# Kernel optimization log

Hardware: AMD Instinct MI355X
Metric: run time of the kernel (lower is better)

Reference implementation:

```python
import jax, jax.numpy as jnp
import numpy as np

B, T_OUT, C, L = 8, 8, 64, 1024  # batch, temporal channels, spatial channels (=in_channels), time steps


def setup_inputs() -> dict:
    key = jax.random.key(0)
    ks = jax.random.split(key, 7)
    s = 1.0 / np.sqrt(C)  # conv1d default init scale
    return {
        "x": jax.random.normal(ks[0], (B, T_OUT, C, L), dtype=jnp.float32),
        "Wq": jax.random.uniform(ks[1], (C, C), jnp.float32, -s, s),
        "bq": jax.random.uniform(ks[2], (C,), jnp.float32, -s, s),
        "Wk": jax.random.uniform(ks[3], (C, C), jnp.float32, -s, s),
        "bk": jax.random.uniform(ks[4], (C,), jnp.float32, -s, s),
        "Wv": jax.random.uniform(ks[5], (C, C), jnp.float32, -s, s),
        "bv": jax.random.uniform(ks[6], (C,), jnp.float32, -s, s),
    }


def reference(x, Wq, bq, Wk, bk, Wv, bv):
    b, t, c, l = x.shape
    xr = x.reshape(b * t, c, l)  # [BT, C, L]
    # 1x1 Conv1d == per-timestep linear over channels
    q = jnp.einsum('oc,bcl->bol', Wq, xr) + bq[:, None]
    k = jnp.einsum('oc,bcl->bol', Wk, xr) + bk[:, None]
    v = jnp.einsum('oc,bcl->bol', Wv, xr) + bv[:, None]
    # scores[b, i, j] = sum_c q[b, c, i] * k[b, c, j]  -> [BT, L, L]
    scores = jnp.einsum('bci,bcj->bij', q, k)
    weights = jax.nn.softmax(scores, axis=-1)
    # out[b, i, c] = sum_j weights[b, i, j] * v[b, c, j]
    out = jnp.einsum('bij,bcj->bic', weights, v)
    out = jnp.transpose(out, (0, 2, 1))  # [BT, C, L]
    return out.reshape(b, t, c, l)
```

## Files before the change

### kernel.cpp

```cpp
#include <hip/hip_runtime.h>

#define CC 64
#define LL 1024
#define LOG2E 1.44269504f

typedef unsigned short u16;
typedef unsigned int u32;
typedef __attribute__((ext_vector_type(8))) short short8;
typedef __attribute__((ext_vector_type(4))) float floatx4;

static __device__ __forceinline__ u16 f2b(float f) {
  return (u16)((__float_as_uint(f) + 0x8000u) >> 16);
}
static __device__ __forceinline__ u32 pk2(float a, float b) {
  return ((__float_as_uint(a) + 0x8000u) >> 16) |
         ((__float_as_uint(b) + 0x8000u) & 0xffff0000u);
}
static __device__ __forceinline__ u32 pk2t(float a, float b) {
  return __builtin_amdgcn_perm(__float_as_uint(b), __float_as_uint(a), 0x07060302u);
}
static __device__ __forceinline__ short8 mk8(u32 a, u32 b, u32 c, u32 d) {
  union { u32 u[4]; short8 s; } t;
  t.u[0] = a; t.u[1] = b; t.u[2] = c; t.u[3] = d;
  return t.s;
}

__global__ __launch_bounds__(256) void w_prep(
    const float* __restrict__ Wq, const float* __restrict__ bq,
    const float* __restrict__ Wk, const float* __restrict__ bk,
    const float* __restrict__ Wv, const float* __restrict__ bv,
    u16* __restrict__ whi, float* __restrict__ bsc)
{
  const int idx = blockIdx.x * 256 + threadIdx.x;
  const int m = idx >> 12;
  const float* W = (m == 0) ? Wq : (m == 1) ? Wk : Wv;
  const float w = W[idx & 4095] * ((m == 0) ? LOG2E : 1.0f);
  whi[idx] = f2b(w);
  if (blockIdx.x == 0 && threadIdx.x < 192)
    bsc[threadIdx.x] = (threadIdx.x < 64) ? bq[threadIdx.x] * LOG2E
                     : (threadIdx.x < 128) ? bk[threadIdx.x - 64] : bv[threadIdx.x - 128];
}

__global__ __launch_bounds__(256) void qkv_kernel(
    const float* __restrict__ x,
    const u16* __restrict__ whi, const float* __restrict__ bsc,
    u16* __restrict__ qT, u16* __restrict__ kT, u16* __restrict__ vO)
{
  __shared__ __align__(16) u16 tbuf_s[4 * 16 * 72];

  const int tid  = threadIdx.x;
  const int wave = tid >> 6;
  const int lane = tid & 63;
  const int l16  = lane & 15;
  const int quad = lane >> 4;

  const int bt = blockIdx.x & 63;
  const int l0 = (blockIdx.x >> 6) << 6;
  const int l  = l0 + wave * 16 + l16;

  const float* xb = x + (size_t)bt * CC * LL + l;
  float xv0[8], xv1[8];
  #pragma unroll
  for (int e = 0; e < 8; ++e) {
    xv0[e] = xb[(size_t)(quad * 8 + e) * LL];
    xv1[e] = xb[(size_t)(quad * 8 + 32 + e) * LL];
  }
  const short8 xh0 = mk8(pk2(xv0[0], xv0[1]), pk2(xv0[2], xv0[3]),
                         pk2(xv0[4], xv0[5]), pk2(xv0[6], xv0[7]));
  const short8 xh1 = mk8(pk2(xv1[0], xv1[1]), pk2(xv1[2], xv1[3]),
                         pk2(xv1[4], xv1[5]), pk2(xv1[6], xv1[7]));

  u16* tb = tbuf_s + wave * 1152;

  #pragma unroll
  for (int ot = 0; ot < 12; ++ot) {
    const int m = ot >> 2;
    const int off = (m << 12) + (((ot & 3) * 16 + l16) << 6) + quad * 8;
    const short8 ah0 = *(const short8*)(whi + off);
    const short8 ah1 = *(const short8*)(whi + off + 32);

    floatx4 acc = (floatx4){0.f, 0.f, 0.f, 0.f};
    acc = __builtin_amdgcn_mfma_f32_16x16x32_bf16(ah0, xh0, acc, 0, 0, 0);
    acc = __builtin_amdgcn_mfma_f32_16x16x32_bf16(ah1, xh1, acc, 0, 0, 0);

    const float4 bb = *(const float4*)(bsc + ot * 16 + quad * 4);
    float ov[4];
    ov[0] = acc[0] + bb.x; ov[1] = acc[1] + bb.y;
    ov[2] = acc[2] + bb.z; ov[3] = acc[3] + bb.w;

    if (ot < 8) {
      uint2 pv;
      pv.x = pk2(ov[0], ov[1]);
      pv.y = pk2(ov[2], ov[3]);
      *(uint2*)(tb + l16 * 72 + (ot & 3) * 16 + quad * 4) = pv;
      if ((ot & 3) == 3) {
        asm volatile("" ::: "memory");
        u16* gdst = ((ot < 4) ? qT : kT) + ((size_t)(bt * LL + l0 + wave * 16)) * CC;
        const int rr = lane >> 3;
        const int c8 = (lane & 7) * 8;
        #pragma unroll
        for (int s2 = 0; s2 < 2; ++s2) {
          const int row = s2 * 8 + rr;
          uint4 val = *(const uint4*)(tb + row * 72 + c8);
          *(uint4*)(gdst + row * CC + c8) = val;
        }
        asm volatile("" ::: "memory");
      }
    } else {
      const int ob = (ot - 8) * 16 + quad * 4;
      u16* vdst = vO + ((size_t)(bt * CC + ob)) * LL + l0 + wave * 16 + l16;
      #pragma unroll
      for (int r = 0; r < 4; ++r)
        vdst[(size_t)r * LL] = f2b(ov[r]);
    }
  }
}

__global__ __launch_bounds__(256) void attn_kernel(
    const u16* __restrict__ qT, const u16* __restrict__ kT,
    const u16* __restrict__ vB, float* __restrict__ out)
{
  __shared__ __align__(16) u16 smem[18432];
  const int tid  = threadIdx.x;
  const int wave = tid >> 6;
  const int lane = tid & 63;
  const int l16  = lane & 15;
  const int quad = lane >> 4;

  const int bt    = blockIdx.x & 63;
  const int chunk = blockIdx.x >> 6;
  const int i0w   = (chunk << 6) + (wave << 4);

  const u16* kbase = kT + (size_t)bt * LL * CC;
  const u16* vbase = vB + (size_t)bt * CC * LL;

  short8 qf[2];
  {
    const u16* qr = qT + (size_t)bt * LL * CC + (size_t)(i0w + l16) * CC + quad * 8;
    qf[0] = *(const short8*)(qr);
    qf[1] = *(const short8*)(qr + 32);
  }

  floatx4 O[4];
  #pragma unroll
  for (int cf = 0; cf < 4; ++cf)
    O[cf] = (floatx4){0.f, 0.f, 0.f, 0.f};
  float lsA = 0.f, lsB = 0.f;

  const int r_st = tid >> 2;
  const int c_st = (tid & 3) << 4;
  const int sr = (r_st & 0x20) | ((r_st & 4) << 2) | ((r_st & 0x18) >> 1) | (r_st & 3);

  {
    uint4 k0 = *(const uint4*)(kbase + (size_t)r_st * CC + c_st);
    uint4 k1 = *(const uint4*)(kbase + (size_t)r_st * CC + c_st + 8);
    uint4 v0 = *(const uint4*)(vbase + (size_t)r_st * LL + c_st);
    uint4 v1 = *(const uint4*)(vbase + (size_t)r_st * LL + c_st + 8);
    *(uint4*)(smem + sr * 72 + c_st)              = k0;
    *(uint4*)(smem + sr * 72 + c_st + 8)          = k1;
    *(uint4*)(smem + 4608 + r_st * 72 + c_st)     = v0;
    *(uint4*)(smem + 4608 + r_st * 72 + c_st + 8) = v1;
  }
  __syncthreads();

  for (int it = 0; it < 16; ++it) {
    u16* ktc = smem + (it & 1) * 9216;
    u16* vtc = ktc + 4608;

    uint4 rk0, rk1, rv0, rv1;
    if (it < 15) {
      const int jb = (it + 1) << 6;
      rk0 = *(const uint4*)(kbase + (size_t)(jb + r_st) * CC + c_st);
      rk1 = *(const uint4*)(kbase + (size_t)(jb + r_st) * CC + c_st + 8);
      rv0 = *(const uint4*)(vbase + (size_t)r_st * LL + jb + c_st);
      rv1 = *(const uint4*)(vbase + (size_t)r_st * LL + jb + c_st + 8);
    }

    floatx4 S[4];
    __builtin_amdgcn_s_setprio(1);
    #pragma unroll
    for (int jt = 0; jt < 4; ++jt) {
      const u16* ka = ktc + (jt * 16 + l16) * 72 + quad * 8;
      const short8 a0 = *(const short8*)(ka);
      const short8 a1 = *(const short8*)(ka + 32);
      floatx4 acc = (floatx4){0.f, 0.f, 0.f, 0.f};
      acc = __builtin_amdgcn_mfma_f32_16x16x32_bf16(a0, qf[0], acc, 0, 0, 0);
      acc = __builtin_amdgcn_mfma_f32_16x16x32_bf16(a1, qf[1], acc, 0, 0, 0);
      S[jt] = acc;
    }
    __builtin_amdgcn_s_setprio(0);

    short8 v0f[4], v1f[4];
    #pragma unroll
    for (int cf = 0; cf < 4; ++cf) {
      const u16* va = vtc + (cf * 16 + l16) * 72 + quad * 8;
      v0f[cf] = *(const short8*)(va);
      v1f[cf] = *(const short8*)(va + 32);
    }

    uint2 pp[4];
    #pragma unroll
    for (int jt = 0; jt < 4; ++jt) {
      const float e0 = __builtin_amdgcn_exp2f(S[jt][0]);
      const float e1 = __builtin_amdgcn_exp2f(S[jt][1]);
      const float e2 = __builtin_amdgcn_exp2f(S[jt][2]);
      const float e3 = __builtin_amdgcn_exp2f(S[jt][3]);
      lsA += e0 + e1;
      lsB += e2 + e3;
      pp[jt].x = pk2t(e0, e1);
      pp[jt].y = pk2t(e2, e3);
    }

    __builtin_amdgcn_s_setprio(1);
    {
      const short8 pa0 = mk8(pp[0].x, pp[0].y, pp[1].x, pp[1].y);
      const short8 pa1 = mk8(pp[2].x, pp[2].y, pp[3].x, pp[3].y);
      #pragma unroll
      for (int cf = 0; cf < 4; ++cf) {
        O[cf] = __builtin_amdgcn_mfma_f32_16x16x32_bf16(pa0, v0f[cf], O[cf], 0, 0, 0);
        O[cf] = __builtin_amdgcn_mfma_f32_16x16x32_bf16(pa1, v1f[cf], O[cf], 0, 0, 0);
      }
    }
    __builtin_amdgcn_s_setprio(0);

    if (it < 15) {
      u16* ktn = smem + ((it + 1) & 1) * 9216;
      *(uint4*)(ktn + sr * 72 + c_st)              = rk0;
      *(uint4*)(ktn + sr * 72 + c_st + 8)          = rk1;
      *(uint4*)(ktn + 4608 + r_st * 72 + c_st)     = rv0;
      *(uint4*)(ktn + 4608 + r_st * 72 + c_st + 8) = rv1;
    }
    __syncthreads();
  }

  float lsum = lsA + lsB;
  lsum += __shfl_xor(lsum, 16, 64);
  lsum += __shfl_xor(lsum, 32, 64);

  __syncthreads();
  float* of = (float*)smem + wave * 1280;
  #pragma unroll
  for (int r = 0; r < 4; ++r) {
    const float rl = __builtin_amdgcn_rcpf(__shfl(lsum, quad * 4 + r, 64));
    #pragma unroll
    for (int cf = 0; cf < 4; ++cf)
      O[cf][r] *= rl;
  }
  asm volatile("" ::: "memory");
  #pragma unroll
  for (int cf = 0; cf < 4; ++cf)
    #pragma unroll
    for (int r = 0; r < 4; ++r)
      of[(cf * 16 + l16) * 20 + quad * 4 + r] = O[cf][r];
  asm volatile("" ::: "memory");
  {
    float* ob = out + ((size_t)bt * CC) * LL + i0w;
    #pragma unroll
    for (int rr = 0; rr < 4; ++rr) {
      const int c = rr * 16 + l16;
      float4 val = *(const float4*)(of + c * 20 + quad * 4);
      *(float4*)(ob + (size_t)c * LL + quad * 4) = val;
    }
  }
  asm volatile("" ::: "memory");
}

extern "C" void kernel_launch(void* const* d_in, const int* in_sizes, int n_in,
                              void* d_out, int out_size, void* d_ws, size_t ws_size,
                              hipStream_t stream) {
  const float* x  = (const float*)d_in[0];
  const float* Wq = (const float*)d_in[1];
  const float* bq = (const float*)d_in[2];
  const float* Wk = (const float*)d_in[3];
  const float* bk = (const float*)d_in[4];
  const float* Wv = (const float*)d_in[5];
  const float* bv = (const float*)d_in[6];
  float* out = (float*)d_out;

  u16* qTp = (u16*)d_ws;
  u16* kTp = qTp + (size_t)64 * LL * CC;
  u16* vp  = kTp + (size_t)64 * LL * CC;
  u16* whi = vp  + (size_t)64 * LL * CC;
  float* bsc = (float*)(whi + 3 * 64 * 64);

  w_prep<<<48, 256, 0, stream>>>(Wq, bq, Wk, bk, Wv, bv, whi, bsc);
  qkv_kernel<<<1024, 256, 0, stream>>>(x, whi, bsc, qTp, kTp, vp);
  attn_kernel<<<1024, 256, 0, stream>>>(qTp, kTp, vp, out);
}
```

Baseline: 123.5 us.

## Fuse QKV projection into attention kernel, recomputing K/V tiles per block

Merges the projection and attention kernels: each 512-thread block projects its own Q rows and recomputes K and V tiles from x directly into shared memory while iterating over keys, prefetching the next x tile. This removes the bf16 Q/K/V workspace writes and reads and one kernel launch. In exchange, K/V projection is redundantly recomputed by every block sharing a batch slice, and x is re-read multiple times with strided fp32 loads.

```diff
diff --git a/kernel.cpp b/kernel.cpp
--- a/kernel.cpp
+++ b/kernel.cpp
@@ -41,12 +41,12 @@
                      : (threadIdx.x < 128) ? bk[threadIdx.x - 64] : bv[threadIdx.x - 128];
 }
 
-__global__ __launch_bounds__(256) void qkv_kernel(
+__global__ __launch_bounds__(512) void fused_kernel(
     const float* __restrict__ x,
     const u16* __restrict__ whi, const float* __restrict__ bsc,
-    u16* __restrict__ qT, u16* __restrict__ kT, u16* __restrict__ vO)
+    float* __restrict__ out)
 {
-  __shared__ __align__(16) u16 tbuf_s[4 * 16 * 72];
+  __shared__ __align__(16) u16 smem[20480];
 
   const int tid  = threadIdx.x;
   const int wave = tid >> 6;
@@ -54,91 +54,47 @@
   const int l16  = lane & 15;
   const int quad = lane >> 4;
 
-  const int bt = blockIdx.x & 63;
-  const int l0 = (blockIdx.x >> 6) << 6;
-  const int l  = l0 + wave * 16 + l16;
-
-  const float* xb = x + (size_t)bt * CC * LL + l;
-  float xv0[8], xv1[8];
-  #pragma unroll
-  for (int e = 0; e < 8; ++e) {
-    xv0[e] = xb[(size_t)(quad * 8 + e) * LL];
-    xv1[e] = xb[(size_t)(quad * 8 + 32 + e) * LL];
-  }
-  const short8 xh0 = mk8(pk2(xv0[0], xv0[1]), pk2(xv0[2], xv0[3]),
-                         pk2(xv0[4], xv0[5]), pk2(xv0[6], xv0[7]));
-  const short8 xh1 = mk8(pk2(xv1[0], xv1[1]), pk2(xv1[2], xv1[3]),
-                         pk2(xv1[4], xv1[5]), pk2(xv1[6], xv1[7]));
-
-  u16* tb = tbuf_s + wave * 1152;
-
-  #pragma unroll
-  for (int ot = 0; ot < 12; ++ot) {
-    const int m = ot >> 2;
-    const int off = (m << 12) + (((ot & 3) * 16 + l16) << 6) + quad * 8;
-    const short8 ah0 = *(const short8*)(whi + off);
-    const short8 ah1 = *(const short8*)(whi + off + 32);
-
-    floatx4 acc = (floatx4){0.f, 0.f, 0.f, 0.f};
-    acc = __builtin_amdgcn_mfma_f32_16x16x32_bf16(ah0, xh0, acc, 0, 0, 0);
-    acc = __builtin_amdgcn_mfma_f32_16x16x32_bf16(ah1, xh1, acc, 0, 0, 0);
-
-    const float4 bb = *(const float4*)(bsc + ot * 16 + quad * 4);
-    float ov[4];
-    ov[0] = acc[0] + bb.x; ov[1] = acc[1] + bb.y;
-    ov[2] = acc[2] + bb.z; ov[3] = acc[3] + bb.w;
-
-    if (ot < 8) {
+  const int bt  = blockIdx.x & 63;
+  const int ih  = blockIdx.x >> 6;
+  const int i0w = (ih << 7) + (wave << 4);
+
+  const int jt  = wave & 3;
+  const int ot0 = (wave >> 2) << 1;
+
+  const float* xbt = x + (size_t)bt * CC * LL;
+
+  short8 qf0, qf1;
+  {
+    const float* xq = xbt + i0w + l16;
+    float qx[16];
+    #pragma unroll
+    for (int e = 0; e < 8; ++e) {
+      qx[e]     = xq[(size_t)(quad * 8 + e) * LL];
+      qx[8 + e] = xq[(size_t)(quad * 8 + 32 + e) * LL];
+    }
+    const short8 qxh0 = mk8(pk2(qx[0], qx[1]), pk2(qx[2], qx[3]),
+                            pk2(qx[4], qx[5]), pk2(qx[6], qx[7]));
+    const short8 qxh1 = mk8(pk2(qx[8], qx[9]), pk2(qx[10], qx[11]),
+                            pk2(qx[12], qx[13]), pk2(qx[14], qx[15]));
+    u16* tb = smem + 9216 + wave * 1152;
+    #pragma unroll
+    for (int ot = 0; ot < 4; ++ot) {
+      const int off = ((ot * 16 + l16) << 6) + quad * 8;
+      const short8 ah0 = *(const short8*)(whi + off);
+      const short8 ah1 = *(const short8*)(whi + off + 32);
+      floatx4 acc = (floatx4){0.f, 0.f, 0.f, 0.f};
+      acc = __builtin_amdgcn_mfma_f32_16x16x32_bf16(ah0, qxh0, acc, 0, 0, 0);
+      acc = __builtin_amdgcn_mfma_f32_16x16x32_bf16(ah1, qxh1, acc, 0, 0, 0);
+      const float4 bb = *(const float4*)(bsc + ot * 16 + quad * 4);
       uint2 pv;
-      pv.x = pk2(ov[0], ov[1]);
-      pv.y = pk2(ov[2], ov[3]);
-      *(uint2*)(tb + l16 * 72 + (ot & 3) * 16 + quad * 4) = pv;
-      if ((ot & 3) == 3) {
-        asm volatile("" ::: "memory");
-        u16* gdst = ((ot < 4) ? qT : kT) + ((size_t)(bt * LL + l0 + wave * 16)) * CC;
-        const int rr = lane >> 3;
-        const int c8 = (lane & 7) * 8;
-        #pragma unroll
-        for (int s2 = 0; s2 < 2; ++s2) {
-          const int row = s2 * 8 + rr;
-          uint4 val = *(const uint4*)(tb + row * 72 + c8);
-          *(uint4*)(gdst + row * CC + c8) = val;
-        }
-        asm volatile("" ::: "memory");
-      }
-    } else {
-      const int ob = (ot - 8) * 16 + quad * 4;
-      u16* vdst = vO + ((size_t)(bt * CC + ob)) * LL + l0 + wave * 16 + l16;
-      #pragma unroll
-      for (int r = 0; r < 4; ++r)
-        vdst[(size_t)r * LL] = f2b(ov[r]);
-    }
-  }
-}
-
-__global__ __launch_bounds__(256) void attn_kernel(
-    const u16* __restrict__ qT, const u16* __restrict__ kT,
-    const u16* __restrict__ vB, float* __restrict__ out)
-{
-  __shared__ __align__(16) u16 smem[18432];
-  const int tid  = threadIdx.x;
-  const int wave = tid >> 6;
-  const int lane = tid & 63;
-  const int l16  = lane & 15;
-  const int quad = lane >> 4;
-
-  const int bt    = blockIdx.x & 63;
-  const int chunk = blockIdx.x >> 6;
-  const int i0w   = (chunk << 6) + (wave << 4);
-
-  const u16* kbase = kT + (size_t)bt * LL * CC;
-  const u16* vbase = vB + (size_t)bt * CC * LL;
-
-  short8 qf[2];
-  {
-    const u16* qr = qT + (size_t)bt * LL * CC + (size_t)(i0w + l16) * CC + quad * 8;
-    qf[0] = *(const short8*)(qr);
-    qf[1] = *(const short8*)(qr + 32);
+      pv.x = pk2(acc[0] + bb.x, acc[1] + bb.y);
+      pv.y = pk2(acc[2] + bb.z, acc[3] + bb.w);
+      *(uint2*)(tb + l16 * 72 + ot * 16 + quad * 4) = pv;
+    }
+    asm volatile("" ::: "memory");
+    qf0 = *(const short8*)(tb + l16 * 72 + quad * 8);
+    qf1 = *(const short8*)(tb + l16 * 72 + quad * 8 + 32);
+    asm volatile("" ::: "memory");
   }
 
   floatx4 O[4];
@@ -147,68 +103,106 @@
     O[cf] = (floatx4){0.f, 0.f, 0.f, 0.f};
   float lsA = 0.f, lsB = 0.f;
 
-  const int r_st = tid >> 2;
-  const int c_st = (tid & 3) << 4;
-  const int sr = (r_st & 0x20) | ((r_st & 4) << 2) | ((r_st & 0x18) >> 1) | (r_st & 3);
+  const int jloc = jt * 16 + l16;
+  const int srow = (jloc & 32) | ((jloc & 4) << 2) | ((jloc & 24) >> 1) | (jloc & 3);
+
+  auto proj = [&](const float (&px)[16], u16* Kb, u16* Vb) {
+    const short8 xh0 = mk8(pk2(px[0], px[1]), pk2(px[2], px[3]),
+                           pk2(px[4], px[5]), pk2(px[6], px[7]));
+    const short8 xh1 = mk8(pk2(px[8], px[9]), pk2(px[10], px[11]),
+                           pk2(px[12], px[13]), pk2(px[14], px[15]));
+    #pragma unroll
+    for (int o2 = 0; o2 < 2; ++o2) {
+      const int ot = ot0 + o2;
+      {
+        const int off = 4096 + ((ot * 16 + l16) << 6) + quad * 8;
+        const short8 ah0 = *(const short8*)(whi + off);
+        const short8 ah1 = *(const short8*)(whi + off + 32);
+        floatx4 acc = (floatx4){0.f, 0.f, 0.f, 0.f};
+        acc = __builtin_amdgcn_mfma_f32_16x16x32_bf16(ah0, xh0, acc, 0, 0, 0);
+        acc = __builtin_amdgcn_mfma_f32_16x16x32_bf16(ah1, xh1, acc, 0, 0, 0);
+        const float4 bb = *(const float4*)(bsc + 64 + ot * 16 + quad * 4);
+        uint2 pv;
+        pv.x = pk2(acc[0] + bb.x, acc[1] + bb.y);
+        pv.y = pk2(acc[2] + bb.z, acc[3] + bb.w);
+        *(uint2*)(Kb + srow * 72 + ot * 16 + quad * 4) = pv;
+      }
+      {
+        const int off = 8192 + ((ot * 16 + l16) << 6) + quad * 8;
+        const short8 ah0 = *(const short8*)(whi + off);
+        const short8 ah1 = *(const short8*)(whi + off + 32);
+        floatx4 acc = (floatx4){0.f, 0.f, 0.f, 0.f};
+        acc = __builtin_amdgcn_mfma_f32_16x16x32_bf16(ah0, xh0, acc, 0, 0, 0);
+        acc = __builtin_amdgcn_mfma_f32_16x16x32_bf16(ah1, xh1, acc, 0, 0, 0);
+        const float4 bb = *(const float4*)(bsc + 128 + ot * 16 + quad * 4);
+        #pragma unroll
+        for (int r = 0; r < 4; ++r) {
+          const float ov = acc[r] + ((const float*)&bb)[r];
+          Vb[(ot * 16 + quad * 4 + r) * 72 + jloc] = f2b(ov);
+        }
+      }
+    }
+  };
 
   {
-    uint4 k0 = *(const uint4*)(kbase + (size_t)r_st * CC + c_st);
-    uint4 k1 = *(const uint4*)(kbase + (size_t)r_st * CC + c_st + 8);
-    uint4 v0 = *(const uint4*)(vbase + (size_t)r_st * LL + c_st);
-    uint4 v1 = *(const uint4*)(vbase + (size_t)r_st * LL + c_st + 8);
-    *(uint4*)(smem + sr * 72 + c_st)              = k0;
-    *(uint4*)(smem + sr * 72 + c_st + 8)          = k1;
-    *(uint4*)(smem + 4608 + r_st * 72 + c_st)     = v0;
-    *(uint4*)(smem + 4608 + r_st * 72 + c_st + 8) = v1;
+    float p0[16];
+    const float* xp = xbt + jt * 16 + l16;
+    #pragma unroll
+    for (int e = 0; e < 8; ++e) {
+      p0[e]     = xp[(size_t)(quad * 8 + e) * LL];
+      p0[8 + e] = xp[(size_t)(quad * 8 + 32 + e) * LL];
+    }
+    proj(p0, smem, smem + 4608);
   }
   __syncthreads();
 
-  for (int it = 0; it < 16; ++it) {
-    u16* ktc = smem + (it & 1) * 9216;
-    u16* vtc = ktc + 4608;
-
-    uint4 rk0, rk1, rv0, rv1;
-    if (it < 15) {
-      const int jb = (it + 1) << 6;
-      rk0 = *(const uint4*)(kbase + (size_t)(jb + r_st) * CC + c_st);
-      rk1 = *(const uint4*)(kbase + (size_t)(jb + r_st) * CC + c_st + 8);
-      rv0 = *(const uint4*)(vbase + (size_t)r_st * LL + jb + c_st);
-      rv1 = *(const uint4*)(vbase + (size_t)r_st * LL + jb + c_st + 8);
+  for (int t = 0; t < 16; ++t) {
+    const u16* Kc = smem + (t & 1) * 9216;
+    const u16* Vc = Kc + 4608;
+
+    float px[16];
+    if (t < 15) {
+      const float* xp = xbt + ((t + 1) << 6) + jt * 16 + l16;
+      #pragma unroll
+      for (int e = 0; e < 8; ++e) {
+        px[e]     = xp[(size_t)(quad * 8 + e) * LL];
+        px[8 + e] = xp[(size_t)(quad * 8 + 32 + e) * LL];
+      }
     }
 
     floatx4 S[4];
     __builtin_amdgcn_s_setprio(1);
     #pragma unroll
-    for (int jt = 0; jt < 4; ++jt) {
-      const u16* ka = ktc + (jt * 16 + l16) * 72 + quad * 8;
+    for (int jt2 = 0; jt2 < 4; ++jt2) {
+      const u16* ka = Kc + (jt2 * 16 + l16) * 72 + quad * 8;
       const short8 a0 = *(const short8*)(ka);
       const short8 a1 = *(const short8*)(ka + 32);
       floatx4 acc = (floatx4){0.f, 0.f, 0.f, 0.f};
-      acc = __builtin_amdgcn_mfma_f32_16x16x32_bf16(a0, qf[0], acc, 0, 0, 0);
-      acc = __builtin_amdgcn_mfma_f32_16x16x32_bf16(a1, qf[1], acc, 0, 0, 0);
-      S[jt] = acc;
+      acc = __builtin_amdgcn_mfma_f32_16x16x32_bf16(a0, qf0, acc, 0, 0, 0);
+      acc = __builtin_amdgcn_mfma_f32_16x16x32_bf16(a1, qf1, acc, 0, 0, 0);
+      S[jt2] = acc;
     }
     __builtin_amdgcn_s_setprio(0);
 
     short8 v0f[4], v1f[4];
     #pragma unroll
     for (int cf = 0; cf < 4; ++cf) {
-      const u16* va = vtc + (cf * 16 + l16) * 72 + quad * 8;
+      const u16* va = Vc + (cf * 16 + l16) * 72 + quad * 8;
       v0f[cf] = *(const short8*)(va);
       v1f[cf] = *(const short8*)(va + 32);
     }
 
     uint2 pp[4];
     #pragma unroll
-    for (int jt = 0; jt < 4; ++jt) {
-      const float e0 = __builtin_amdgcn_exp2f(S[jt][0]);
-      const float e1 = __builtin_amdgcn_exp2f(S[jt][1]);
-      const float e2 = __builtin_amdgcn_exp2f(S[jt][2]);
-      const float e3 = __builtin_amdgcn_exp2f(S[jt][3]);
+    for (int jt2 = 0; jt2 < 4; ++jt2) {
+      const float e0 = __builtin_amdgcn_exp2f(S[jt2][0]);
+      const float e1 = __builtin_amdgcn_exp2f(S[jt2][1]);
+      const float e2 = __builtin_amdgcn_exp2f(S[jt2][2]);
+      const float e3 = __builtin_amdgcn_exp2f(S[jt2][3]);
       lsA += e0 + e1;
       lsB += e2 + e3;
-      pp[jt].x = pk2t(e0, e1);
-      pp[jt].y = pk2t(e2, e3);
+      pp[jt2].x = pk2t(e0, e1);
+      pp[jt2].y = pk2t(e2, e3);
     }
 
     __builtin_amdgcn_s_setprio(1);
@@ -223,12 +217,9 @@
     }
     __builtin_amdgcn_s_setprio(0);
 
-    if (it < 15) {
-      u16* ktn = smem + ((it + 1) & 1) * 9216;
-      *(uint4*)(ktn + sr * 72 + c_st)              = rk0;
-      *(uint4*)(ktn + sr * 72 + c_st + 8)          = rk1;
-      *(uint4*)(ktn + 4608 + r_st * 72 + c_st)     = rv0;
-      *(uint4*)(ktn + 4608 + r_st * 72 + c_st + 8) = rv1;
+    if (t < 15) {
+      u16* Kn = smem + ((t + 1) & 1) * 9216;
+      proj(px, Kn, Kn + 4608);
     }
     __syncthreads();
   }
@@ -237,8 +228,7 @@
   lsum += __shfl_xor(lsum, 16, 64);
   lsum += __shfl_xor(lsum, 32, 64);
 
-  __syncthreads();
-  float* of = (float*)smem + wave * 1280;
+  float* ofw = (float*)smem + wave * 1280;
   #pragma unroll
   for (int r = 0; r < 4; ++r) {
     const float rl = __builtin_amdgcn_rcpf(__shfl(lsum, quad * 4 + r, 64));
@@ -251,14 +241,14 @@
   for (int cf = 0; cf < 4; ++cf)
     #pragma unroll
     for (int r = 0; r < 4; ++r)
-      of[(cf * 16 + l16) * 20 + quad * 4 + r] = O[cf][r];
+      ofw[(cf * 16 + l16) * 20 + quad * 4 + r] = O[cf][r];
   asm volatile("" ::: "memory");
   {
-    float* ob = out + ((size_t)bt * CC) * LL + i0w;
+    float* ob = out + (size_t)bt * CC * LL + i0w;
     #pragma unroll
     for (int rr = 0; rr < 4; ++rr) {
       const int c = rr * 16 + l16;
-      float4 val = *(const float4*)(of + c * 20 + quad * 4);
+      float4 val = *(const float4*)(ofw + c * 20 + quad * 4);
       *(float4*)(ob + (size_t)c * LL + quad * 4) = val;
     }
   }
@@ -277,13 +267,9 @@
   const float* bv = (const float*)d_in[6];
   float* out = (float*)d_out;
 
-  u16* qTp = (u16*)d_ws;
-  u16* kTp = qTp + (size_t)64 * LL * CC;
-  u16* vp  = kTp + (size_t)64 * LL * CC;
-  u16* whi = vp  + (size_t)64 * LL * CC;
+  u16* whi = (u16*)d_ws;
   float* bsc = (float*)(whi + 3 * 64 * 64);
 
   w_prep<<<48, 256, 0, stream>>>(Wq, bq, Wk, bk, Wv, bv, whi, bsc);
-  qkv_kernel<<<1024, 256, 0, stream>>>(x, whi, bsc, qTp, kTp, vp);
-  attn_kernel<<<1024, 256, 0, stream>>>(qTp, kTp, vp, out);
-}
+  fused_kernel<<<512, 512, 0, stream>>>(x, whi, bsc, out);
+}
```

New measurement: 129.1 us. 4.5% more time.
